# Kernel optimization log

Measured on AMD Instinct MI355X. Metric: run time of the kernel, lower is better.

## Reference

```python
import jax, jax.numpy as jnp
import numpy as np

# static config (matches init_kwargs / input_specs)
B, S, D, H, DH = 4, 2048, 2048, 16, 128
MAX_LEN = 1024  # round_up_to_multiple_of_256(max ragged length); lengths below max at 1024
ROPE_BASE = 10000.0


def setup_inputs() -> dict:
    key = jax.random.key(0)
    ks = jax.random.split(key, 8)
    q_src = jax.random.normal(ks[0], (B, MAX_LEN, D), jnp.float32)
    k_src = jax.random.normal(ks[1], (B, S, D), jnp.float32)
    v_src = jax.random.normal(ks[2], (B, S, D), jnp.float32)
    std = 1.0 / np.sqrt(D)
    Wq = jax.random.normal(ks[3], (D, H * DH), jnp.float32) * std
    Wk = jax.random.normal(ks[4], (D, H * DH), jnp.float32) * std
    Wv = jax.random.normal(ks[5], (D, H * DH), jnp.float32) * std
    Wo = jax.random.normal(ks[6], (H * DH, D), jnp.float32) * (1.0 / np.sqrt(H * DH))
    # mask[0]: causal bool [B,S,S]; mask[1]: full position ids [B,S]
    mask0 = jnp.broadcast_to(jnp.tril(jnp.ones((S, S), bool)), (B, S, S))
    pos_full = jnp.broadcast_to(jnp.arange(S, dtype=jnp.int32), (B, S))
    # ragged skip_mask: row i keeps lengths[i] random positions (max 1024 -> MAX_LEN)
    lengths = jnp.array([1024, 896, 768, 640], jnp.int32)
    scores = jax.random.uniform(ks[7], (B, S))
    ranks = jnp.argsort(jnp.argsort(scores, axis=1), axis=1)
    skip_mask = ranks < lengths[:, None]
    return {"q_src": q_src, "k_src": k_src, "v_src": v_src,
            "Wq": Wq, "Wk": Wk, "Wv": Wv, "Wo": Wo,
            "mask0": mask0, "pos_full": pos_full, "skip_mask": skip_mask}


def _rope(x, positions):
    # x: [B,H,L,DH], positions: [B,L] int -> rotary embedding on full head dim
    dh = x.shape[-1]
    inv_freq = 1.0 / (ROPE_BASE ** (jnp.arange(0, dh, 2, dtype=jnp.float32) / dh))
    freqs = positions.astype(jnp.float32)[:, :, None] * inv_freq      # [B,L,dh/2]
    emb = jnp.concatenate([freqs, freqs], axis=-1)[:, None]           # [B,1,L,dh]
    x1, x2 = jnp.split(x, 2, axis=-1)
    rot = jnp.concatenate([-x2, x1], axis=-1)                         # rotate_half
    return x * jnp.cos(emb) + rot * jnp.sin(emb)


def reference(q_src, k_src, v_src, Wq, Wk, Wv, Wo, mask0, pos_full, skip_mask):
    def heads(x, W):
        y = x @ W
        return y.reshape(x.shape[0], x.shape[1], H, DH).transpose(0, 2, 1, 3)

    q = heads(q_src, Wq)   # [B,H,MAX_LEN,DH]
    k = heads(k_src, Wk)   # [B,H,S,DH]
    v = heads(v_src, Wv)   # [B,H,S,DH]

    # _trim_attention_mask: gather kept rows (True-first, stable order), pad to MAX_LEN
    order = jnp.argsort(jnp.where(skip_mask, 0, 1), axis=1)[:, :MAX_LEN]  # [B,MAX_LEN]
    n = skip_mask.sum(axis=1)                                             # ragged lengths
    valid = jnp.arange(MAX_LEN)[None, :] < n[:, None]                     # [B,MAX_LEN]
    amask = jnp.take_along_axis(mask0, order[:, :, None], axis=1) & valid[:, :, None]
    pos_trim = jnp.where(valid, jnp.take_along_axis(pos_full, order, axis=1), 0)

    # RoPE: trimmed positions for q, full positions for k
    q = _rope(q, pos_trim)
    k = _rope(k, pos_full)

    # masked SDPA; fully-masked (padded) query rows -> zero output
    logits = jnp.einsum('bhld,bhsd->bhls', q, k) / np.sqrt(DH).astype(np.float32)
    logits = jnp.where(amask[:, None], logits, jnp.finfo(logits.dtype).min)
    probs = jax.nn.softmax(logits, axis=-1) * valid[:, None, :, None]
    ctx = jnp.einsum('bhls,bhsd->bhld', probs, v)                         # [B,H,MAX_LEN,DH]

    out = ctx.transpose(0, 2, 1, 3).reshape(B, MAX_LEN, H * DH) @ Wo     # [B,MAX_LEN,D]
    return out
```

## Files before the change

kernel.cpp:

```cpp
#include <hip/hip_runtime.h>

#define BB 4
#define SS 2048
#define DD 2048
#define HH 16
#define DHD 128
#define MAXL 1024

typedef __bf16 bf16x8 __attribute__((ext_vector_type(8)));
typedef float f32x4 __attribute__((ext_vector_type(4)));
typedef unsigned int u32_as1 __attribute__((address_space(1)));
typedef unsigned int u32_as3 __attribute__((address_space(3)));

__device__ __forceinline__ unsigned short f2bf(float f) {
  unsigned int u = __builtin_bit_cast(unsigned int, f);
  u += 0x7fffu + ((u >> 16) & 1u);
  return (unsigned short)(u >> 16);
}
__device__ __forceinline__ float bf2f(unsigned short h) {
  unsigned int u = ((unsigned int)h) << 16;
  return __builtin_bit_cast(float, u);
}
union U4 { uint4 u; bf16x8 b; };
__device__ __forceinline__ bf16x8 ldfrag(const unsigned short* p) {
  U4 x; x.u = *(const uint4*)p; return x.b;
}
__device__ __forceinline__ void gl_lds16(const void* g, void* l) {
  __builtin_amdgcn_global_load_lds((const u32_as1*)g, (u32_as3*)l, 16, 0, 0);
}

__global__ void build_pos(const int* __restrict__ skip, int* __restrict__ posk,
                          int* __restrict__ nval) {
  int b = blockIdx.x, t = threadIdx.x;
  __shared__ int cnts[64], offs[64];
  const int* row = skip + b * SS;
  int c = 0;
  for (int i = 0; i < 32; i++) c += (row[t * 32 + i] != 0);
  cnts[t] = c;
  __syncthreads();
  if (t == 0) {
    int run = 0;
    for (int i = 0; i < 64; i++) { offs[i] = run; run += cnts[i]; }
    nval[b] = run > MAXL ? MAXL : run;
  }
  __syncthreads();
  int o = offs[t];
  for (int i = 0; i < 32; i++)
    if (row[t * 32 + i]) { if (o < MAXL) posk[b * MAXL + o] = t * 32 + i; o++; }
  int nb = nval[b];
  for (int l = nb + t; l < MAXL; l += 64) posk[b * MAXL + l] = -1;
}

__global__ __launch_bounds__(256) void cvt_bf16(const float* __restrict__ in,
                                                unsigned short* __restrict__ out, int n) {
  int idx = (blockIdx.x * 256 + threadIdx.x) * 4;
  int stride = gridDim.x * 256 * 4;
  for (; idx < n; idx += stride) {
    float4 v = *(const float4*)&in[idx];
    ushort4 h;
    h.x = f2bf(v.x); h.y = f2bf(v.y); h.z = f2bf(v.z); h.w = f2bf(v.w);
    *(ushort4*)&out[idx] = h;
  }
}

__global__ __launch_bounds__(256) void transpose_bf16(const float* __restrict__ W,
                                                      unsigned short* __restrict__ Wt,
                                                      int Kdim, int Ndim) {
  __shared__ __align__(16) unsigned short tile[64 * 76];
  int tx = threadIdx.x;
  int K0 = blockIdx.y * 64, N0 = blockIdx.x * 64;
  #pragma unroll
  for (int i = 0; i < 4; i++) {
    int r = (tx >> 4) + i * 16;
    int c4 = (tx & 15) * 4;
    float4 v = *(const float4*)&W[(size_t)(K0 + r) * Ndim + N0 + c4];
    ushort4 h;
    h.x = f2bf(v.x); h.y = f2bf(v.y); h.z = f2bf(v.z); h.w = f2bf(v.w);
    *(ushort4*)&tile[r * 76 + c4] = h;
  }
  __syncthreads();
  #pragma unroll
  for (int i = 0; i < 4; i++) {
    int n = (tx >> 4) + i * 16;
    int k4 = (tx & 15) * 4;
    ushort4 h;
    h.x = tile[(k4 + 0) * 76 + n];
    h.y = tile[(k4 + 1) * 76 + n];
    h.z = tile[(k4 + 2) * 76 + n];
    h.w = tile[(k4 + 3) * 76 + n];
    *(ushort4*)&Wt[(size_t)(N0 + n) * Kdim + K0 + k4] = h;
  }
}

__global__ __launch_bounds__(256) void gemm_bt(const unsigned short* __restrict__ A,
                                               const unsigned short* __restrict__ Bt,
                                               void* __restrict__ Cp,
                                               int M, int N, int K, int mode, int Lbits) {
  __shared__ __align__(16) unsigned short As[128 * 32];
  __shared__ __align__(16) unsigned short Bs[128 * 32];
  const int tid = threadIdx.x;
  const int lane = tid & 63, quad = lane >> 4, c = lane & 15;
  const int w = tid >> 6;
  const int wm = (w >> 1) * 64, wn = (w & 1) * 64;
  const size_t tm = (size_t)blockIdx.y * 128, tn = (size_t)blockIdx.x * 128;

  f32x4 acc[4][4] = {};

  const int srow = tid >> 2, scol = (tid & 3) * 8;
  const unsigned short* ga = A + (tm + srow) * K + scol;
  const unsigned short* gb = Bt + (tn + srow) * K + scol;
  unsigned short* la = &As[tid * 8];
  unsigned short* lb = &Bs[tid * 8];

  for (int kk = 0; kk < K; kk += 32) {
    gl_lds16(ga + kk, la);
    gl_lds16(ga + kk + (size_t)64 * K, la + 2048);
    gl_lds16(gb + kk, lb);
    gl_lds16(gb + kk + (size_t)64 * K, lb + 2048);
    __syncthreads();
    bf16x8 af[4], bfr[4];
    #pragma unroll
    for (int i = 0; i < 4; i++) af[i] = ldfrag(&As[(wm + i * 16 + c) * 32 + quad * 8]);
    #pragma unroll
    for (int j = 0; j < 4; j++) bfr[j] = ldfrag(&Bs[(wn + j * 16 + c) * 32 + quad * 8]);
    #pragma unroll
    for (int i = 0; i < 4; i++)
      #pragma unroll
      for (int j = 0; j < 4; j++)
        acc[i][j] = __builtin_amdgcn_mfma_f32_16x16x32_bf16(af[i], bfr[j], acc[i][j], 0, 0, 0);
    __syncthreads();
  }

  if (mode == 0) {
    unsigned short* Cb = (unsigned short*)Cp;
    const size_t Lmask = ((size_t)1 << Lbits) - 1;
    #pragma unroll
    for (int i = 0; i < 4; i++)
      #pragma unroll
      for (int j = 0; j < 4; j++)
        #pragma unroll
        for (int r = 0; r < 4; r++) {
          size_t m = tm + wm + i * 16 + quad * 4 + r;
          size_t n = tn + wn + j * 16 + c;
          size_t b = m >> Lbits, l = m & Lmask;
          size_t h = n >> 7, d = n & 127;
          Cb[(((b * HH + h) << Lbits) + l) * 128 + d] = f2bf(acc[i][j][r]);
        }
  } else {
    float* Cf = (float*)Cp;
    #pragma unroll
    for (int i = 0; i < 4; i++)
      #pragma unroll
      for (int j = 0; j < 4; j++)
        #pragma unroll
        for (int r = 0; r < 4; r++) {
          size_t m = tm + wm + i * 16 + quad * 4 + r;
          size_t n = tn + wn + j * 16 + c;
          Cf[m * N + n] = acc[i][j][r];
        }
  }
}

__global__ __launch_bounds__(256) void rope_kernel(unsigned short* __restrict__ x,
                                                   const int* __restrict__ posk,
                                                   int Lbits, int use_posk) {
  int idx = blockIdx.x * 256 + threadIdx.x;
  int d = idx & 63;
  int rest = idx >> 6;
  int l = rest & ((1 << Lbits) - 1);
  int bh = rest >> Lbits;
  int b = bh >> 4;
  int p = use_posk ? posk[(b << 10) + l] : l;
  float ang = (float)p * __expf(-(float)d * 0.14391156831212787f);
  float sn, cs;
  __sincosf(ang, &sn, &cs);
  size_t base = (size_t)rest * 128;
  float x1 = bf2f(x[base + d]), x2 = bf2f(x[base + d + 64]);
  x[base + d]      = f2bf(x1 * cs - x2 * sn);
  x[base + d + 64] = f2bf(x2 * cs + x1 * sn);
}

__global__ __launch_bounds__(256) void attn_kernel(const unsigned short* __restrict__ qp,
                                                   const unsigned short* __restrict__ kp,
                                                   const unsigned short* __restrict__ vp,
                                                   const int* __restrict__ posk,
                                                   const int* __restrict__ nval,
                                                   unsigned short* __restrict__ ctx) {
  __shared__ __align__(16) unsigned short q_s[64 * 136];
  __shared__ __align__(16) unsigned short k_s[64 * 136];
  __shared__ __align__(16) unsigned short vt_s[128 * 72];
  __shared__ __align__(16) unsigned short p_s[4 * 16 * 72];
  __shared__ int km_s[64];

  const int tid = threadIdx.x;
  const int w = tid >> 6, lane = tid & 63, quad = lane >> 4, c = lane & 15;
  const int bh = blockIdx.y, b = bh >> 4, h = bh & 15;
  const int qbase = blockIdx.x * 64;
  const int nb = nval[b];

  const unsigned short* qg = qp + (((size_t)bh << 10) + qbase) * 128;
  const unsigned short* kg = kp + ((size_t)bh << 11) * 128;
  const unsigned short* vg = vp + ((size_t)bh << 11) * 128;

  if (tid < 64) {
    int l = qbase + tid;
    km_s[tid] = (l < nb) ? posk[(b << 10) + l] : -1;
  }
  {
    int r = tid >> 4, c8 = (tid & 15) * 8;
    #pragma unroll
    for (int i = 0; i < 4; i++)
      *(uint4*)&q_s[(r + i * 16) * 136 + c8] = *(const uint4*)&qg[(size_t)(r + i * 16) * 128 + c8];
  }
  __syncthreads();

  int lv = nb - 1 - qbase; lv = lv > 63 ? 63 : lv;
  const int tile_kmax = (lv >= 0) ? km_s[lv] : -1;
  const int nkt = (tile_kmax >= 0) ? ((tile_kmax >> 6) + 1) : 0;

  int km[4];
  #pragma unroll
  for (int r = 0; r < 4; r++) km[r] = km_s[w * 16 + quad * 4 + r];

  float m_i[4], l_i[4];
  #pragma unroll
  for (int r = 0; r < 4; r++) { m_i[r] = -1e30f; l_i[r] = 0.f; }
  f32x4 o[8];
  #pragma unroll
  for (int dj = 0; dj < 8; dj++) o[dj] = (f32x4){0.f, 0.f, 0.f, 0.f};

  for (int kt = 0; kt < nkt; kt++) {
    const int kb = kt * 64;
    __syncthreads();
    {
      int r = tid >> 4, c8 = (tid & 15) * 8;
      #pragma unroll
      for (int i = 0; i < 4; i++)
        *(uint4*)&k_s[(r + i * 16) * 136 + c8] =
            *(const uint4*)&kg[(size_t)(kb + r + i * 16) * 128 + c8];
      int s = tid & 63, dbase = (tid >> 6) * 8;
      #pragma unroll
      for (int i = 0; i < 4; i++) {
        int d0 = dbase + i * 32;
        uint4 vv = *(const uint4*)&vg[(size_t)(kb + s) * 128 + d0];
        unsigned short* ep = (unsigned short*)&vv;
        #pragma unroll
        for (int j = 0; j < 8; j++) vt_s[(d0 + j) * 72 + s] = ep[j];
      }
    }
    __syncthreads();

    bf16x8 aq[4];
    #pragma unroll
    for (int ks = 0; ks < 4; ks++) aq[ks] = ldfrag(&q_s[(w * 16 + c) * 136 + ks * 32 + quad * 8]);
    f32x4 sa[4];
    #pragma unroll
    for (int j = 0; j < 4; j++) {
      sa[j] = (f32x4){0.f, 0.f, 0.f, 0.f};
      #pragma unroll
      for (int ks = 0; ks < 4; ks++) {
        bf16x8 bk = ldfrag(&k_s[(j * 16 + c) * 136 + ks * 32 + quad * 8]);
        sa[j] = __builtin_amdgcn_mfma_f32_16x16x32_bf16(aq[ks], bk, sa[j], 0, 0, 0);
      }
    }

    const float scale = 0.08838834764831843f;
    float mt[4] = {-1e30f, -1e30f, -1e30f, -1e30f};
    #pragma unroll
    for (int j = 0; j < 4; j++) {
      int key = kb + j * 16 + c;
      #pragma unroll
      for (int r = 0; r < 4; r++) {
        float v = (key <= km[r]) ? sa[j][r] * scale : -1e30f;
        sa[j][r] = v;
        mt[r] = fmaxf(mt[r], v);
      }
    }
    #pragma unroll
    for (int r = 0; r < 4; r++)
      for (int off = 1; off < 16; off <<= 1)
        mt[r] = fmaxf(mt[r], __shfl_xor(mt[r], off, 16));
    float al[4], rs[4];
    #pragma unroll
    for (int r = 0; r < 4; r++) {
      float mn = fmaxf(m_i[r], mt[r]);
      al[r] = __expf(m_i[r] - mn);
      m_i[r] = mn;
      rs[r] = 0.f;
    }
    #pragma unroll
    for (int j = 0; j < 4; j++)
      #pragma unroll
      for (int r = 0; r < 4; r++) {
        float pv = __expf(sa[j][r] - m_i[r]);
        sa[j][r] = pv;
        rs[r] += pv;
      }
    #pragma unroll
    for (int r = 0; r < 4; r++) {
      for (int off = 1; off < 16; off <<= 1) rs[r] += __shfl_xor(rs[r], off, 16);
      l_i[r] = l_i[r] * al[r] + rs[r];
    }
    #pragma unroll
    for (int dj = 0; dj < 8; dj++)
      #pragma unroll
      for (int r = 0; r < 4; r++) o[dj][r] *= al[r];

    #pragma unroll
    for (int j = 0; j < 4; j++)
      #pragma unroll
      for (int r = 0; r < 4; r++)
        p_s[w * 1152 + (quad * 4 + r) * 72 + j * 16 + c] = f2bf(sa[j][r]);

    #pragma unroll
    for (int ks2 = 0; ks2 < 2; ks2++) {
      bf16x8 ap = ldfrag(&p_s[w * 1152 + c * 72 + ks2 * 32 + quad * 8]);
      #pragma unroll
      for (int dj = 0; dj < 8; dj++) {
        bf16x8 bv = ldfrag(&vt_s[(dj * 16 + c) * 72 + ks2 * 32 + quad * 8]);
        o[dj] = __builtin_amdgcn_mfma_f32_16x16x32_bf16(ap, bv, o[dj], 0, 0, 0);
      }
    }
  }

  #pragma unroll
  for (int r = 0; r < 4; r++) {
    int l = qbase + w * 16 + quad * 4 + r;
    bool ok = (l < nb);
    float inv = ok ? (1.0f / l_i[r]) : 0.0f;
    #pragma unroll
    for (int dj = 0; dj < 8; dj++)
      ctx[(((size_t)b << 10) + l) * (size_t)DD + h * 128 + dj * 16 + c] =
          f2bf(ok ? o[dj][r] * inv : 0.0f);
  }
}

extern "C" void kernel_launch(void* const* d_in, const int* in_sizes, int n_in,
                              void* d_out, int out_size, void* d_ws, size_t ws_size,
                              hipStream_t stream) {
  const float* q_src = (const float*)d_in[0];
  const float* k_src = (const float*)d_in[1];
  const float* v_src = (const float*)d_in[2];
  const float* Wq = (const float*)d_in[3];
  const float* Wk = (const float*)d_in[4];
  const float* Wv = (const float*)d_in[5];
  const float* Wo = (const float*)d_in[6];
  const int* skip = (const int*)d_in[9];

  char* p = (char*)d_ws;
  auto alloc = [&](size_t bytes) -> char* {
    char* r = p;
    p += (bytes + 255) & ~(size_t)255;
    return r;
  };
  unsigned short* a_q  = (unsigned short*)alloc((size_t)BB * MAXL * DD * 2);
  unsigned short* a_k  = (unsigned short*)alloc((size_t)BB * SS * DD * 2);
  unsigned short* a_v  = (unsigned short*)alloc((size_t)BB * SS * DD * 2);
  unsigned short* wt_q = (unsigned short*)alloc((size_t)DD * DD * 2);
  unsigned short* wt_k = (unsigned short*)alloc((size_t)DD * DD * 2);
  unsigned short* wt_v = (unsigned short*)alloc((size_t)DD * DD * 2);
  unsigned short* wt_o = (unsigned short*)alloc((size_t)DD * DD * 2);
  unsigned short* q_pro = (unsigned short*)alloc((size_t)BB * HH * MAXL * DHD * 2);
  unsigned short* k_pro = (unsigned short*)alloc((size_t)BB * HH * SS * DHD * 2);
  unsigned short* v_pro = (unsigned short*)alloc((size_t)BB * HH * SS * DHD * 2);
  int* posk = (int*)alloc((size_t)BB * MAXL * 4);
  int* nval = (int*)alloc(64);
  unsigned short* ctx = a_q;

  build_pos<<<BB, 64, 0, stream>>>(skip, posk, nval);
  cvt_bf16<<<4096, 256, 0, stream>>>(q_src, a_q, BB * MAXL * DD);
  cvt_bf16<<<4096, 256, 0, stream>>>(k_src, a_k, BB * SS * DD);
  cvt_bf16<<<4096, 256, 0, stream>>>(v_src, a_v, BB * SS * DD);
  transpose_bf16<<<dim3(32, 32), 256, 0, stream>>>(Wq, wt_q, DD, DD);
  transpose_bf16<<<dim3(32, 32), 256, 0, stream>>>(Wk, wt_k, DD, DD);
  transpose_bf16<<<dim3(32, 32), 256, 0, stream>>>(Wv, wt_v, DD, DD);
  transpose_bf16<<<dim3(32, 32), 256, 0, stream>>>(Wo, wt_o, DD, DD);

  gemm_bt<<<dim3(16, 32), 256, 0, stream>>>(a_q, wt_q, q_pro, BB * MAXL, DD, DD, 0, 10);
  gemm_bt<<<dim3(16, 64), 256, 0, stream>>>(a_k, wt_k, k_pro, BB * SS, DD, DD, 0, 11);
  gemm_bt<<<dim3(16, 64), 256, 0, stream>>>(a_v, wt_v, v_pro, BB * SS, DD, DD, 0, 11);

  rope_kernel<<<(BB * HH * MAXL * 64) / 256, 256, 0, stream>>>(q_pro, posk, 10, 1);
  rope_kernel<<<(BB * HH * SS * 64) / 256, 256, 0, stream>>>(k_pro, posk, 11, 0);

  attn_kernel<<<dim3(MAXL / 64, BB * HH), 256, 0, stream>>>(q_pro, k_pro, v_pro, posk, nval, ctx);

  gemm_bt<<<dim3(16, 32), 256, 0, stream>>>(ctx, wt_o, d_out, BB * MAXL, DD, DD, 1, 0);
}
```

Baseline: 843.7 us.

## Fuse prep kernels, stage GEMM epilogues through LDS, pre-transpose V for attention

Merges the three input conversions into one launch, the four weight transposes into one, and the two RoPE passes into one, cutting launch count. The GEMM epilogue now stages results in LDS so global stores are 16-byte vectors. A new mode writes V already transposed, which lets attention load K and V^T straight into XOR-swizzled LDS with direct global-to-LDS copies instead of a scalar in-LDS transpose. Attention also keeps Q fragments in registers loaded once, and its grid is reordered so blocks sharing a batch-head run together. The cost is more epilogue complexity, and the V^T write is a strided-by-SS store pattern.

```diff
diff --git a/kernel.cpp b/kernel.cpp
--- a/kernel.cpp
+++ b/kernel.cpp
@@ -51,29 +51,42 @@
   for (int l = nb + t; l < MAXL; l += 64) posk[b * MAXL + l] = -1;
 }
 
-__global__ __launch_bounds__(256) void cvt_bf16(const float* __restrict__ in,
-                                                unsigned short* __restrict__ out, int n) {
-  int idx = (blockIdx.x * 256 + threadIdx.x) * 4;
-  int stride = gridDim.x * 256 * 4;
-  for (; idx < n; idx += stride) {
-    float4 v = *(const float4*)&in[idx];
-    ushort4 h;
-    h.x = f2bf(v.x); h.y = f2bf(v.y); h.z = f2bf(v.z); h.w = f2bf(v.w);
-    *(ushort4*)&out[idx] = h;
-  }
-}
-
-__global__ __launch_bounds__(256) void transpose_bf16(const float* __restrict__ W,
-                                                      unsigned short* __restrict__ Wt,
-                                                      int Kdim, int Ndim) {
+__global__ __launch_bounds__(256) void cvt3(const float* __restrict__ q,
+                                            const float* __restrict__ k,
+                                            const float* __restrict__ v,
+                                            unsigned short* __restrict__ oq,
+                                            unsigned short* __restrict__ ok,
+                                            unsigned short* __restrict__ ov) {
+  const int nq = BB * MAXL * DD / 4, nk = BB * SS * DD / 4;
+  int idx = blockIdx.x * 256 + threadIdx.x;
+  const float* src; unsigned short* dst; int off;
+  if (idx < nq) { src = q; dst = oq; off = idx; }
+  else if (idx < nq + nk) { src = k; dst = ok; off = idx - nq; }
+  else { src = v; dst = ov; off = idx - nq - nk; }
+  float4 vv = ((const float4*)src)[off];
+  ushort4 h;
+  h.x = f2bf(vv.x); h.y = f2bf(vv.y); h.z = f2bf(vv.z); h.w = f2bf(vv.w);
+  ((ushort4*)dst)[off] = h;
+}
+
+__global__ __launch_bounds__(256) void transpose_w4(const float* __restrict__ w0,
+    const float* __restrict__ w1, const float* __restrict__ w2, const float* __restrict__ w3,
+    unsigned short* __restrict__ o0, unsigned short* __restrict__ o1,
+    unsigned short* __restrict__ o2, unsigned short* __restrict__ o3) {
   __shared__ __align__(16) unsigned short tile[64 * 76];
+  const float* W; unsigned short* Wt;
+  switch (blockIdx.z) {
+    case 0: W = w0; Wt = o0; break;
+    case 1: W = w1; Wt = o1; break;
+    case 2: W = w2; Wt = o2; break;
+    default: W = w3; Wt = o3; break;
+  }
   int tx = threadIdx.x;
   int K0 = blockIdx.y * 64, N0 = blockIdx.x * 64;
   #pragma unroll
   for (int i = 0; i < 4; i++) {
-    int r = (tx >> 4) + i * 16;
-    int c4 = (tx & 15) * 4;
-    float4 v = *(const float4*)&W[(size_t)(K0 + r) * Ndim + N0 + c4];
+    int r = (tx >> 4) + i * 16, c4 = (tx & 15) * 4;
+    float4 v = *(const float4*)&W[(size_t)(K0 + r) * DD + N0 + c4];
     ushort4 h;
     h.x = f2bf(v.x); h.y = f2bf(v.y); h.z = f2bf(v.z); h.w = f2bf(v.w);
     *(ushort4*)&tile[r * 76 + c4] = h;
@@ -81,14 +94,13 @@
   __syncthreads();
   #pragma unroll
   for (int i = 0; i < 4; i++) {
-    int n = (tx >> 4) + i * 16;
-    int k4 = (tx & 15) * 4;
+    int n = (tx >> 4) + i * 16, k4 = (tx & 15) * 4;
     ushort4 h;
     h.x = tile[(k4 + 0) * 76 + n];
     h.y = tile[(k4 + 1) * 76 + n];
     h.z = tile[(k4 + 2) * 76 + n];
     h.w = tile[(k4 + 3) * 76 + n];
-    *(ushort4*)&Wt[(size_t)(N0 + n) * Kdim + K0 + k4] = h;
+    *(ushort4*)&Wt[(size_t)(N0 + n) * DD + K0 + k4] = h;
   }
 }
 
@@ -96,8 +108,9 @@
                                                const unsigned short* __restrict__ Bt,
                                                void* __restrict__ Cp,
                                                int M, int N, int K, int mode, int Lbits) {
-  __shared__ __align__(16) unsigned short As[128 * 32];
-  __shared__ __align__(16) unsigned short Bs[128 * 32];
+  __shared__ __align__(16) unsigned short buf[4 * 4352];
+  unsigned short* As = buf;
+  unsigned short* Bs = buf + 4096;
   const int tid = threadIdx.x;
   const int lane = tid & 63, quad = lane >> 4, c = lane & 15;
   const int w = tid >> 6;
@@ -131,22 +144,7 @@
     __syncthreads();
   }
 
-  if (mode == 0) {
-    unsigned short* Cb = (unsigned short*)Cp;
-    const size_t Lmask = ((size_t)1 << Lbits) - 1;
-    #pragma unroll
-    for (int i = 0; i < 4; i++)
-      #pragma unroll
-      for (int j = 0; j < 4; j++)
-        #pragma unroll
-        for (int r = 0; r < 4; r++) {
-          size_t m = tm + wm + i * 16 + quad * 4 + r;
-          size_t n = tn + wn + j * 16 + c;
-          size_t b = m >> Lbits, l = m & Lmask;
-          size_t h = n >> 7, d = n & 127;
-          Cb[(((b * HH + h) << Lbits) + l) * 128 + d] = f2bf(acc[i][j][r]);
-        }
-  } else {
+  if (mode == 1) {
     float* Cf = (float*)Cp;
     #pragma unroll
     for (int i = 0; i < 4; i++)
@@ -158,13 +156,56 @@
           size_t n = tn + wn + j * 16 + c;
           Cf[m * N + n] = acc[i][j][r];
         }
-  }
-}
-
-__global__ __launch_bounds__(256) void rope_kernel(unsigned short* __restrict__ x,
-                                                   const int* __restrict__ posk,
-                                                   int Lbits, int use_posk) {
-  int idx = blockIdx.x * 256 + threadIdx.x;
+    return;
+  }
+  unsigned short* Cb = (unsigned short*)Cp;
+  unsigned short* ep = buf + w * 4352;
+  if (mode == 0) {
+    #pragma unroll
+    for (int i = 0; i < 4; i++)
+      #pragma unroll
+      for (int j = 0; j < 4; j++)
+        #pragma unroll
+        for (int r = 0; r < 4; r++)
+          ep[(i * 16 + quad * 4 + r) * 68 + j * 16 + c] = f2bf(acc[i][j][r]);
+    const size_t Lmask = ((size_t)1 << Lbits) - 1;
+    #pragma unroll
+    for (int it = 0; it < 8; it++) {
+      int chunk = it * 64 + lane;
+      int ml = chunk >> 3, nc = (chunk & 7) * 8;
+      uint4 val = *(const uint4*)&ep[ml * 68 + nc];
+      size_t m = tm + wm + ml, n = tn + wn + nc;
+      size_t b = m >> Lbits, l = m & Lmask, h = n >> 7, d = n & 127;
+      *(uint4*)&Cb[(((b * HH + h) << Lbits) + l) * 128 + d] = val;
+    }
+  } else {
+    #pragma unroll
+    for (int i = 0; i < 4; i++)
+      #pragma unroll
+      for (int j = 0; j < 4; j++)
+        #pragma unroll
+        for (int r = 0; r < 4; r++)
+          ep[(j * 16 + c) * 68 + i * 16 + quad * 4 + r] = f2bf(acc[i][j][r]);
+    #pragma unroll
+    for (int it = 0; it < 8; it++) {
+      int chunk = it * 64 + lane;
+      int nl = chunk >> 3, mc = (chunk & 7) * 8;
+      uint4 val = *(const uint4*)&ep[nl * 68 + mc];
+      size_t n = tn + wn + nl, m = tm + wm + mc;
+      size_t b = m >> 11, s = m & 2047, h = n >> 7, d = n & 127;
+      *(uint4*)&Cb[((b * HH + h) * 128 + d) * SS + s] = val;
+    }
+  }
+}
+
+__global__ __launch_bounds__(256) void rope2(unsigned short* __restrict__ xq,
+                                             unsigned short* __restrict__ xk,
+                                             const int* __restrict__ posk) {
+  const int Nq = BB * HH * MAXL * 64;
+  int gid = blockIdx.x * 256 + threadIdx.x;
+  unsigned short* x; int Lbits, idx, use_posk;
+  if (gid < Nq) { x = xq; Lbits = 10; use_posk = 1; idx = gid; }
+  else { x = xk; Lbits = 11; use_posk = 0; idx = gid - Nq; }
   int d = idx & 63;
   int rest = idx >> 6;
   int l = rest & ((1 << Lbits) - 1);
@@ -182,37 +223,32 @@
 
 __global__ __launch_bounds__(256) void attn_kernel(const unsigned short* __restrict__ qp,
                                                    const unsigned short* __restrict__ kp,
-                                                   const unsigned short* __restrict__ vp,
+                                                   const unsigned short* __restrict__ vtp,
                                                    const int* __restrict__ posk,
                                                    const int* __restrict__ nval,
                                                    unsigned short* __restrict__ ctx) {
-  __shared__ __align__(16) unsigned short q_s[64 * 136];
-  __shared__ __align__(16) unsigned short k_s[64 * 136];
-  __shared__ __align__(16) unsigned short vt_s[128 * 72];
+  __shared__ __align__(16) unsigned short k_s[64 * 128];
+  __shared__ __align__(16) unsigned short vt_s[128 * 64];
   __shared__ __align__(16) unsigned short p_s[4 * 16 * 72];
   __shared__ int km_s[64];
 
   const int tid = threadIdx.x;
   const int w = tid >> 6, lane = tid & 63, quad = lane >> 4, c = lane & 15;
-  const int bh = blockIdx.y, b = bh >> 4, h = bh & 15;
-  const int qbase = blockIdx.x * 64;
+  const int bh = blockIdx.x, b = bh >> 4, h = bh & 15;
+  const int qbase = blockIdx.y * 64;
   const int nb = nval[b];
-
-  const unsigned short* qg = qp + (((size_t)bh << 10) + qbase) * 128;
-  const unsigned short* kg = kp + ((size_t)bh << 11) * 128;
-  const unsigned short* vg = vp + ((size_t)bh << 11) * 128;
 
   if (tid < 64) {
     int l = qbase + tid;
     km_s[tid] = (l < nb) ? posk[(b << 10) + l] : -1;
   }
-  {
-    int r = tid >> 4, c8 = (tid & 15) * 8;
-    #pragma unroll
-    for (int i = 0; i < 4; i++)
-      *(uint4*)&q_s[(r + i * 16) * 136 + c8] = *(const uint4*)&qg[(size_t)(r + i * 16) * 128 + c8];
-  }
   __syncthreads();
+
+  const unsigned short* qg = qp + (((size_t)bh << 10) + qbase) * 128;
+  bf16x8 aq[4];
+  #pragma unroll
+  for (int ks = 0; ks < 4; ks++)
+    aq[ks] = ldfrag(&qg[(size_t)(w * 16 + c) * 128 + ks * 32 + quad * 8]);
 
   int lv = nb - 1 - qbase; lv = lv > 63 ? 63 : lv;
   const int tile_kmax = (lv >= 0) ? km_s[lv] : -1;
@@ -222,6 +258,13 @@
   #pragma unroll
   for (int r = 0; r < 4; r++) km[r] = km_s[w * 16 + quad * 4 + r];
 
+  const int srow = tid >> 4;
+  const int kswz = (tid & 15) ^ (srow & 7);
+  const unsigned short* kgp = kp + ((size_t)bh << 11) * 128 + (size_t)srow * 128 + kswz * 8;
+  const int dvrow = tid >> 3;
+  const int vswz = (tid & 7) ^ (dvrow & 7);
+  const unsigned short* vgp = vtp + ((size_t)bh * 128 + dvrow) * SS + vswz * 8;
+
   float m_i[4], l_i[4];
   #pragma unroll
   for (int r = 0; r < 4; r++) { m_i[r] = -1e30f; l_i[r] = 0.f; }
@@ -232,34 +275,21 @@
   for (int kt = 0; kt < nkt; kt++) {
     const int kb = kt * 64;
     __syncthreads();
-    {
-      int r = tid >> 4, c8 = (tid & 15) * 8;
-      #pragma unroll
-      for (int i = 0; i < 4; i++)
-        *(uint4*)&k_s[(r + i * 16) * 136 + c8] =
-            *(const uint4*)&kg[(size_t)(kb + r + i * 16) * 128 + c8];
-      int s = tid & 63, dbase = (tid >> 6) * 8;
-      #pragma unroll
-      for (int i = 0; i < 4; i++) {
-        int d0 = dbase + i * 32;
-        uint4 vv = *(const uint4*)&vg[(size_t)(kb + s) * 128 + d0];
-        unsigned short* ep = (unsigned short*)&vv;
-        #pragma unroll
-        for (int j = 0; j < 8; j++) vt_s[(d0 + j) * 72 + s] = ep[j];
-      }
-    }
+    #pragma unroll
+    for (int i = 0; i < 4; i++)
+      gl_lds16(kgp + ((size_t)kb + i * 16) * 128, &k_s[(i * 256 + tid) * 8]);
+    #pragma unroll
+    for (int i = 0; i < 4; i++)
+      gl_lds16(vgp + (size_t)kb + (size_t)i * 32 * SS, &vt_s[(i * 256 + tid) * 8]);
     __syncthreads();
 
-    bf16x8 aq[4];
-    #pragma unroll
-    for (int ks = 0; ks < 4; ks++) aq[ks] = ldfrag(&q_s[(w * 16 + c) * 136 + ks * 32 + quad * 8]);
     f32x4 sa[4];
     #pragma unroll
     for (int j = 0; j < 4; j++) {
       sa[j] = (f32x4){0.f, 0.f, 0.f, 0.f};
       #pragma unroll
       for (int ks = 0; ks < 4; ks++) {
-        bf16x8 bk = ldfrag(&k_s[(j * 16 + c) * 136 + ks * 32 + quad * 8]);
+        bf16x8 bk = ldfrag(&k_s[((j * 16 + c) << 7) + (((ks * 4 + quad) ^ (c & 7)) << 3)]);
         sa[j] = __builtin_amdgcn_mfma_f32_16x16x32_bf16(aq[ks], bk, sa[j], 0, 0, 0);
       }
     }
@@ -317,7 +347,7 @@
       bf16x8 ap = ldfrag(&p_s[w * 1152 + c * 72 + ks2 * 32 + quad * 8]);
       #pragma unroll
       for (int dj = 0; dj < 8; dj++) {
-        bf16x8 bv = ldfrag(&vt_s[(dj * 16 + c) * 72 + ks2 * 32 + quad * 8]);
+        bf16x8 bv = ldfrag(&vt_s[((dj * 16 + c) << 6) + (((ks2 * 4 + quad) ^ (c & 7)) << 3)]);
         o[dj] = __builtin_amdgcn_mfma_f32_16x16x32_bf16(ap, bv, o[dj], 0, 0, 0);
       }
     }
@@ -362,28 +392,23 @@
   unsigned short* wt_o = (unsigned short*)alloc((size_t)DD * DD * 2);
   unsigned short* q_pro = (unsigned short*)alloc((size_t)BB * HH * MAXL * DHD * 2);
   unsigned short* k_pro = (unsigned short*)alloc((size_t)BB * HH * SS * DHD * 2);
-  unsigned short* v_pro = (unsigned short*)alloc((size_t)BB * HH * SS * DHD * 2);
+  unsigned short* v_t   = (unsigned short*)alloc((size_t)BB * HH * SS * DHD * 2);
   int* posk = (int*)alloc((size_t)BB * MAXL * 4);
   int* nval = (int*)alloc(64);
   unsigned short* ctx = a_q;
 
   build_pos<<<BB, 64, 0, stream>>>(skip, posk, nval);
-  cvt_bf16<<<4096, 256, 0, stream>>>(q_src, a_q, BB * MAXL * DD);
-  cvt_bf16<<<4096, 256, 0, stream>>>(k_src, a_k, BB * SS * DD);
-  cvt_bf16<<<4096, 256, 0, stream>>>(v_src, a_v, BB * SS * DD);
-  transpose_bf16<<<dim3(32, 32), 256, 0, stream>>>(Wq, wt_q, DD, DD);
-  transpose_bf16<<<dim3(32, 32), 256, 0, stream>>>(Wk, wt_k, DD, DD);
-  transpose_bf16<<<dim3(32, 32), 256, 0, stream>>>(Wv, wt_v, DD, DD);
-  transpose_bf16<<<dim3(32, 32), 256, 0, stream>>>(Wo, wt_o, DD, DD);
+  cvt3<<<(BB * MAXL * DD + 2 * BB * SS * DD) / (4 * 256), 256, 0, stream>>>(
+      q_src, k_src, v_src, a_q, a_k, a_v);
+  transpose_w4<<<dim3(32, 32, 4), 256, 0, stream>>>(Wq, Wk, Wv, Wo, wt_q, wt_k, wt_v, wt_o);
 
   gemm_bt<<<dim3(16, 32), 256, 0, stream>>>(a_q, wt_q, q_pro, BB * MAXL, DD, DD, 0, 10);
   gemm_bt<<<dim3(16, 64), 256, 0, stream>>>(a_k, wt_k, k_pro, BB * SS, DD, DD, 0, 11);
-  gemm_bt<<<dim3(16, 64), 256, 0, stream>>>(a_v, wt_v, v_pro, BB * SS, DD, DD, 0, 11);
-
-  rope_kernel<<<(BB * HH * MAXL * 64) / 256, 256, 0, stream>>>(q_pro, posk, 10, 1);
-  rope_kernel<<<(BB * HH * SS * 64) / 256, 256, 0, stream>>>(k_pro, posk, 11, 0);
-
-  attn_kernel<<<dim3(MAXL / 64, BB * HH), 256, 0, stream>>>(q_pro, k_pro, v_pro, posk, nval, ctx);
+  gemm_bt<<<dim3(16, 64), 256, 0, stream>>>(a_v, wt_v, v_t, BB * SS, DD, DD, 2, 11);
+
+  rope2<<<(BB * HH * (MAXL + SS) * 64) / 256, 256, 0, stream>>>(q_pro, k_pro, posk);
+
+  attn_kernel<<<dim3(BB * HH, MAXL / 64), 256, 0, stream>>>(q_pro, k_pro, v_t, posk, nval, ctx);
 
   gemm_bt<<<dim3(16, 32), 256, 0, stream>>>(ctx, wt_o, d_out, BB * MAXL, DD, DD, 1, 0);
 }
```

Result: faster. 762.1 us (-9.7%).
